# Kernel tuning notes

Measured on AMD Instinct MI355X. Metric: run time of the kernel, lower is better.

The kernel has to match this reference:

```python
import jax, jax.numpy as jnp
import numpy as np

N_NODES = 100000
N_EDGES = 1600000
IN_DIM = 64
OUT_DIM = 64


def setup_inputs() -> dict:
    key = jax.random.key(0)
    ks = jax.random.split(key, 8)
    features = jax.random.normal(ks[0], (N_NODES, IN_DIM), dtype=jnp.float32)
    q_w = jax.random.normal(ks[1], (IN_DIM, IN_DIM), dtype=jnp.float32) * 0.05
    q_b = jnp.zeros((IN_DIM,), dtype=jnp.float32)
    w_w = jax.random.normal(ks[2], (2 * IN_DIM, OUT_DIM), dtype=jnp.float32) * 0.05
    w_b = jnp.zeros((OUT_DIM,), dtype=jnp.float32)
    alpha = jax.random.uniform(ks[3], (N_EDGES,), dtype=jnp.float32)
    src = jax.random.randint(ks[4], (N_EDGES,), 0, N_NODES, dtype=jnp.int32)
    dst = jax.random.randint(ks[5], (N_EDGES,), 0, N_NODES, dtype=jnp.int32)
    return {"features": features, "q_w": q_w, "q_b": q_b,
            "w_w": w_w, "w_b": w_b, "alpha": alpha, "src": src, "dst": dst}


def reference(features, q_w, q_b, w_w, w_b, alpha, src, dst):
    # h = ReLU(q(features)) -- projected features for both src and dst nodes
    h = jax.nn.relu(features @ q_w + q_b)                      # [N, in_dim]
    # edge-weighted messages: u_mul_e('h','alpha') then sum by dst
    msgs = h[src] * alpha[:, None]                             # [E, in_dim]
    h_n = jax.ops.segment_sum(msgs, dst, num_segments=features.shape[0])  # [N, in_dim]
    # concat + linear + ReLU
    z = jax.nn.relu(jnp.concatenate([h, h_n], axis=-1) @ w_w + w_b)       # [N, out_dim]
    # L2 normalize (torch.norm default p=2)
    return z / jnp.linalg.norm(z, axis=-1, keepdims=True)
```

## Files before the change

kernel.cpp:

```cpp
#include <hip/hip_runtime.h>
#include <hip/hip_bf16.h>

#define IN_DIM 64
#define OUT_DIM 64

typedef float nt_f4 __attribute__((ext_vector_type(4)));

__global__ void canary_kernel(int* __restrict__ offsets, int n, int nE) {
    if (threadIdx.x == 0 && blockIdx.x == 0) offsets[n] = nE;
}

__global__ __launch_bounds__(256) void proj_kernel(
    const float4* __restrict__ feat4, const float4* __restrict__ qw4,
    const float4* __restrict__ qb4, float4* __restrict__ h4,
    int* __restrict__ counts, int n) {
    const size_t gtid = blockIdx.x * (size_t)256 + threadIdx.x;
    const int rg   = (int)(gtid >> 2);
    const int sub  = (int)(gtid & 3);
    const int row0 = rg * 4;
    if (row0 >= n) return;
    const int rmax = (n - row0 < 4) ? (n - row0) : 4;

    float4 acc[4][4];
    #pragma unroll
    for (int r = 0; r < 4; ++r)
        #pragma unroll
        for (int m = 0; m < 4; ++m) acc[r][m] = qb4[sub * 4 + m];

    for (int k4 = 0; k4 < 16; ++k4) {
        float4 xv[4];
        #pragma unroll
        for (int r = 0; r < 4; ++r) {
            const int rr = (r < rmax) ? r : 0;
            xv[r] = feat4[(size_t)(row0 + rr) * 16 + k4];
        }
        float4 w[4][4];
        #pragma unroll
        for (int j = 0; j < 4; ++j)
            #pragma unroll
            for (int m = 0; m < 4; ++m)
                w[j][m] = qw4[(k4 * 4 + j) * 16 + sub * 4 + m];
        #pragma unroll
        for (int j = 0; j < 4; ++j) {
            #pragma unroll
            for (int r = 0; r < 4; ++r) {
                const float xs = (j == 0) ? xv[r].x : (j == 1) ? xv[r].y
                               : (j == 2) ? xv[r].z : xv[r].w;
                #pragma unroll
                for (int m = 0; m < 4; ++m) {
                    acc[r][m].x = fmaf(xs, w[j][m].x, acc[r][m].x);
                    acc[r][m].y = fmaf(xs, w[j][m].y, acc[r][m].y);
                    acc[r][m].z = fmaf(xs, w[j][m].z, acc[r][m].z);
                    acc[r][m].w = fmaf(xs, w[j][m].w, acc[r][m].w);
                }
            }
        }
    }

    #pragma unroll
    for (int r = 0; r < 4; ++r) {
        if (r >= rmax) break;
        if (sub == 0) counts[row0 + r] = 0;
        #pragma unroll
        for (int m = 0; m < 4; ++m) {
            float4 v = acc[r][m];
            v.x = fmaxf(v.x, 0.f); v.y = fmaxf(v.y, 0.f);
            v.z = fmaxf(v.z, 0.f); v.w = fmaxf(v.w, 0.f);
            h4[(size_t)(row0 + r) * 16 + sub * 4 + m] = v;
        }
    }
}

__global__ __launch_bounds__(256) void count_kernel(
    const int* __restrict__ dst, int* __restrict__ counts, int n, int nE) {
    const int e = blockIdx.x * 256 + threadIdx.x;
    if (e >= nE) return;
    int d = __builtin_nontemporal_load(&dst[e]);
    d = ((unsigned)d < (unsigned)n) ? d : 0;
    atomicAdd(&counts[d], 1);
}

__global__ __launch_bounds__(256) void scan1_kernel(
    const int* __restrict__ counts, int* __restrict__ offsets,
    int* __restrict__ blocksums, int n) {
    __shared__ int s[256];
    const int tid = threadIdx.x;
    const int i = blockIdx.x * 256 + tid;
    const int v = (i < n) ? counts[i] : 0;
    s[tid] = v;
    __syncthreads();
    #pragma unroll
    for (int off = 1; off < 256; off <<= 1) {
        const int t = (tid >= off) ? s[tid - off] : 0;
        __syncthreads();
        s[tid] += t;
        __syncthreads();
    }
    if (i < n) offsets[i] = s[tid] - v;
    if (tid == 255) blocksums[blockIdx.x] = s[255];
}

__global__ __launch_bounds__(512) void scan2_kernel(int* __restrict__ blocksums, int nb) {
    __shared__ int s[512];
    const int tid = threadIdx.x;
    const int v = (tid < nb) ? blocksums[tid] : 0;
    s[tid] = v;
    __syncthreads();
    #pragma unroll
    for (int off = 1; off < 512; off <<= 1) {
        const int t = (tid >= off) ? s[tid - off] : 0;
        __syncthreads();
        s[tid] += t;
        __syncthreads();
    }
    if (tid < nb) blocksums[tid] = s[tid] - v;
}

__global__ __launch_bounds__(256) void scan3_kernel(
    int* __restrict__ offsets, int* __restrict__ cursor,
    const int* __restrict__ blocksums, int n, int nE) {
    const int i = blockIdx.x * 256 + threadIdx.x;
    if (i < n) {
        const int o = offsets[i] + blocksums[blockIdx.x];
        offsets[i] = o;
        cursor[i]  = o;
    }
    if (i == 0) offsets[n] = nE;
}

__global__ __launch_bounds__(256) void fill_kernel(
    const int* __restrict__ dst, const int* __restrict__ src,
    const float* __restrict__ alpha, int* __restrict__ cursor,
    int2* __restrict__ edges_s, int n, int nE) {
    const int e = blockIdx.x * 256 + threadIdx.x;
    if (e >= nE) return;
    int d = __builtin_nontemporal_load(&dst[e]);
    d = ((unsigned)d < (unsigned)n) ? d : 0;
    const int s = __builtin_nontemporal_load(&src[e]);
    const float a = __builtin_nontemporal_load(&alpha[e]);
    const int p = atomicAdd(&cursor[d], 1);
    if ((unsigned)p < (unsigned)nE) {
        edges_s[p] = make_int2(s, __float_as_int(a));
    }
}

__global__ __launch_bounds__(256) void agg_kernel(
    const float4* __restrict__ h4, const int2* __restrict__ edges_s,
    const int* __restrict__ offsets, float4* __restrict__ hn4, int n, int nE) {
    const size_t gtid = blockIdx.x * (size_t)256 + threadIdx.x;
    const int v    = (int)(gtid >> 6);
    const int lane = (int)(gtid & 63);
    const int q    = lane >> 4;
    const int c4   = lane & 15;
    if (v >= n) return;

    int b  = offsets[v];
    int e1 = offsets[v + 1];
    if (b < 0) b = 0;
    if (e1 > nE) e1 = nE;

    float4 acc = make_float4(0.f, 0.f, 0.f, 0.f);
    for (int j = b + q; j < e1; j += 4) {
        const int2 ed = edges_s[j];
        int s = ed.x;
        s = ((unsigned)s < (unsigned)n) ? s : 0;
        const float a = __int_as_float(ed.y);
        const float4 hv = h4[(size_t)s * 16 + c4];
        acc.x = fmaf(hv.x, a, acc.x);
        acc.y = fmaf(hv.y, a, acc.y);
        acc.z = fmaf(hv.z, a, acc.z);
        acc.w = fmaf(hv.w, a, acc.w);
    }
    acc.x += __shfl_xor(acc.x, 16, 64); acc.y += __shfl_xor(acc.y, 16, 64);
    acc.z += __shfl_xor(acc.z, 16, 64); acc.w += __shfl_xor(acc.w, 16, 64);
    acc.x += __shfl_xor(acc.x, 32, 64); acc.y += __shfl_xor(acc.y, 32, 64);
    acc.z += __shfl_xor(acc.z, 32, 64); acc.w += __shfl_xor(acc.w, 32, 64);

    if (q == 0) hn4[(size_t)v * 16 + c4] = acc;
}

__global__ __launch_bounds__(256) void zero_kernel(float* __restrict__ p, size_t cnt) {
    const size_t i = blockIdx.x * (size_t)256 + threadIdx.x;
    if (i < cnt) p[i] = 0.f;
}
__global__ __launch_bounds__(256) void scatter_kernel(
    const float4* __restrict__ h4, const float* __restrict__ alpha,
    const int* __restrict__ src, const int* __restrict__ dst,
    float* __restrict__ hn, int nE) {
    const size_t gtid = blockIdx.x * (size_t)256 + threadIdx.x;
    const int eid = (int)(gtid >> 4);
    const int c4  = (int)(gtid & 15);
    if (eid >= nE) return;
    const int   s = src[eid];
    const int   d = dst[eid];
    const float a = alpha[eid];
    const float4 v = h4[(size_t)s * 16 + c4];
    float* p = &hn[(size_t)d * IN_DIM + c4 * 4];
    unsafeAtomicAdd(p + 0, v.x * a);
    unsafeAtomicAdd(p + 1, v.y * a);
    unsafeAtomicAdd(p + 2, v.z * a);
    unsafeAtomicAdd(p + 3, v.w * a);
}

__global__ __launch_bounds__(256) void out_kernel(
    const float4* __restrict__ h4, const float4* __restrict__ hn4,
    const float4* __restrict__ ww4, const float4* __restrict__ wb4,
    float4* __restrict__ out4, int n) {
    const size_t gtid = blockIdx.x * (size_t)256 + threadIdx.x;
    const int rg   = (int)(gtid >> 2);
    const int sub  = (int)(gtid & 3);
    const int row0 = rg * 4;
    if (row0 >= n) return;
    const int rmax = (n - row0 < 4) ? (n - row0) : 4;

    float4 acc[4][4];
    #pragma unroll
    for (int r = 0; r < 4; ++r)
        #pragma unroll
        for (int m = 0; m < 4; ++m) acc[r][m] = wb4[sub * 4 + m];

    #pragma unroll
    for (int ph = 0; ph < 2; ++ph) {
        const float4* __restrict__ x4 = (ph == 0) ? h4 : hn4;
        for (int k4 = 0; k4 < 16; ++k4) {
            float4 xv[4];
            #pragma unroll
            for (int r = 0; r < 4; ++r) {
                const int rr = (r < rmax) ? r : 0;
                xv[r] = x4[(size_t)(row0 + rr) * 16 + k4];
            }
            float4 w[4][4];
            #pragma unroll
            for (int j = 0; j < 4; ++j)
                #pragma unroll
                for (int m = 0; m < 4; ++m)
                    w[j][m] = ww4[(ph * 64 + k4 * 4 + j) * 16 + sub * 4 + m];
            #pragma unroll
            for (int j = 0; j < 4; ++j) {
                #pragma unroll
                for (int r = 0; r < 4; ++r) {
                    const float xs = (j == 0) ? xv[r].x : (j == 1) ? xv[r].y
                                   : (j == 2) ? xv[r].z : xv[r].w;
                    #pragma unroll
                    for (int m = 0; m < 4; ++m) {
                        acc[r][m].x = fmaf(xs, w[j][m].x, acc[r][m].x);
                        acc[r][m].y = fmaf(xs, w[j][m].y, acc[r][m].y);
                        acc[r][m].z = fmaf(xs, w[j][m].z, acc[r][m].z);
                        acc[r][m].w = fmaf(xs, w[j][m].w, acc[r][m].w);
                    }
                }
            }
        }
    }

    float sq[4];
    #pragma unroll
    for (int r = 0; r < 4; ++r) {
        float s = 0.f;
        #pragma unroll
        for (int m = 0; m < 4; ++m) {
            acc[r][m].x = fmaxf(acc[r][m].x, 0.f);
            acc[r][m].y = fmaxf(acc[r][m].y, 0.f);
            acc[r][m].z = fmaxf(acc[r][m].z, 0.f);
            acc[r][m].w = fmaxf(acc[r][m].w, 0.f);
            s = fmaf(acc[r][m].x, acc[r][m].x, s);
            s = fmaf(acc[r][m].y, acc[r][m].y, s);
            s = fmaf(acc[r][m].z, acc[r][m].z, s);
            s = fmaf(acc[r][m].w, acc[r][m].w, s);
        }
        sq[r] = s;
    }
    #pragma unroll
    for (int r = 0; r < 4; ++r) {
        sq[r] += __shfl_xor(sq[r], 1, 64);
        sq[r] += __shfl_xor(sq[r], 2, 64);
    }

    #pragma unroll
    for (int r = 0; r < 4; ++r) {
        if (r >= rmax) break;
        const float inv = 1.0f / sqrtf(sq[r]);
        #pragma unroll
        for (int m = 0; m < 4; ++m) {
            nt_f4 v;
            v.x = acc[r][m].x * inv; v.y = acc[r][m].y * inv;
            v.z = acc[r][m].z * inv; v.w = acc[r][m].w * inv;
            __builtin_nontemporal_store(
                v, (nt_f4*)&out4[(size_t)(row0 + r) * 16 + sub * 4 + m]);
        }
    }
}

extern "C" void kernel_launch(void* const* d_in, const int* in_sizes, int n_in,
                              void* d_out, int out_size, void* d_ws, size_t ws_size,
                              hipStream_t stream) {
    const float* feat  = (const float*)d_in[0];
    const float* qw    = (const float*)d_in[1];
    const float* qb    = (const float*)d_in[2];
    const float* ww    = (const float*)d_in[3];
    const float* wb    = (const float*)d_in[4];
    const float* alpha = (const float*)d_in[5];
    const int*   src   = (const int*)d_in[6];
    const int*   dst   = (const int*)d_in[7];
    float* out = (float*)d_out;

    const int n  = in_sizes[0] / IN_DIM;
    const int nE = in_sizes[5];
    const int NB = (n + 255) / 256;

    float* h        = (float*)d_ws;
    float* hn       = h + (size_t)n * IN_DIM;
    int*   counts   = (int*)(hn + (size_t)n * IN_DIM);
    int*   offsets  = counts + n;
    int*   cursor   = offsets + (n + 1);
    int*   blocksums= cursor + n;
    char*  raw      = (char*)(blocksums + NB);
    int2*  edges_s  = (int2*)(((uintptr_t)raw + 7) & ~(uintptr_t)7);
    const size_t needed = (size_t)((char*)(edges_s + nE) - (char*)d_ws);
    const bool do_csr = ws_size >= needed;

    canary_kernel<<<1, 64, 0, stream>>>(offsets, n, nE);

    {
        const long long t = ((long long)(n + 3) / 4) * 4;
        proj_kernel<<<(int)((t + 255) / 256), 256, 0, stream>>>(
            (const float4*)feat, (const float4*)qw, (const float4*)qb,
            (float4*)h, counts, n);
    }

    if (do_csr) {
        count_kernel<<<(nE + 255) / 256, 256, 0, stream>>>(dst, counts, n, nE);
        scan1_kernel<<<NB, 256, 0, stream>>>(counts, offsets, blocksums, n);
        scan2_kernel<<<1, 512, 0, stream>>>(blocksums, NB);
        scan3_kernel<<<NB, 256, 0, stream>>>(offsets, cursor, blocksums, n, nE);
        fill_kernel<<<(nE + 255) / 256, 256, 0, stream>>>(
            dst, src, alpha, cursor, edges_s, n, nE);
        agg_kernel<<<(int)(((long long)n * 64 + 255) / 256), 256, 0, stream>>>(
            (const float4*)h, edges_s, offsets, (float4*)hn, n, nE);
    } else {
        const size_t cnt = (size_t)n * IN_DIM;
        zero_kernel<<<(int)((cnt + 255) / 256), 256, 0, stream>>>(hn, cnt);
        scatter_kernel<<<(int)(((long long)nE * 16 + 255) / 256), 256, 0, stream>>>(
            (const float4*)h, alpha, src, dst, hn, nE);
    }

    {
        const long long t = ((long long)(n + 3) / 4) * 4;
        out_kernel<<<(int)((t + 255) / 256), 256, 0, stream>>>(
            (const float4*)h, (const float4*)hn, (const float4*)ww,
            (const float4*)wb, (float4*)out, n);
    }
}
```

Baseline: 450.0 us.

## Two-pass bucketed partition for CSR fill to localize atomics and scatters

Replaces the single-pass edge fill with a two-stage partition. First, each block bins 4096 edges by coarse destination bucket (512 nodes per bucket) in shared memory and writes them contiguously into a temporary buffer, packing dst, src and a truncated alpha into 64 bits. A second pass then scatters from bucket-ordered records, so the per-node cursor atomics and edge writes hit localized memory regions. This adds an extra pass over the edges and a lossy alpha encoding (low 2 mantissa bits dropped, 17-bit indices). It also reuses the hn buffer as scratch and removes the nontemporal loads.

```diff
diff --git a/kernel.cpp b/kernel.cpp
--- a/kernel.cpp
+++ b/kernel.cpp
@@ -3,8 +3,11 @@
 
 #define IN_DIM 64
 #define OUT_DIM 64
+#define EPB 4096
+#define BSHIFT 9
 
 typedef float nt_f4 __attribute__((ext_vector_type(4)));
+typedef unsigned long long u64;
 
 __global__ void canary_kernel(int* __restrict__ offsets, int n, int nE) {
     if (threadIdx.x == 0 && blockIdx.x == 0) offsets[n] = nE;
@@ -75,7 +78,7 @@
     const int* __restrict__ dst, int* __restrict__ counts, int n, int nE) {
     const int e = blockIdx.x * 256 + threadIdx.x;
     if (e >= nE) return;
-    int d = __builtin_nontemporal_load(&dst[e]);
+    int d = dst[e];
     d = ((unsigned)d < (unsigned)n) ? d : 0;
     atomicAdd(&counts[d], 1);
 }
@@ -118,14 +121,93 @@
 
 __global__ __launch_bounds__(256) void scan3_kernel(
     int* __restrict__ offsets, int* __restrict__ cursor,
-    const int* __restrict__ blocksums, int n, int nE) {
+    const int* __restrict__ blocksums, int* __restrict__ bcur,
+    int n, int nE) {
     const int i = blockIdx.x * 256 + threadIdx.x;
     if (i < n) {
         const int o = offsets[i] + blocksums[blockIdx.x];
         offsets[i] = o;
         cursor[i]  = o;
+        if ((i & ((1 << BSHIFT) - 1)) == 0) bcur[i >> BSHIFT] = o;
     }
     if (i == 0) offsets[n] = nE;
+}
+
+__global__ __launch_bounds__(256) void partA_kernel(
+    const int* __restrict__ dst, const int* __restrict__ src,
+    const float* __restrict__ alpha, int* __restrict__ bcur,
+    u64* __restrict__ tmp, int n, int nE, int nbuk) {
+    __shared__ int hist[256];
+    __shared__ int lofs[256];
+    __shared__ int lcur[256];
+    __shared__ int gbase[256];
+    __shared__ u64 stage[EPB];
+    __shared__ unsigned short sbuk[EPB];
+
+    const int tid = threadIdx.x;
+    const int e0  = blockIdx.x * EPB;
+    const int cnt = (nE - e0 < EPB) ? (nE - e0) : EPB;
+
+    hist[tid] = 0;
+    __syncthreads();
+
+    for (int i = tid; i < cnt; i += 256) {
+        int d = dst[e0 + i];
+        d = ((unsigned)d < (unsigned)n) ? d : 0;
+        atomicAdd(&hist[d >> BSHIFT], 1);
+    }
+    __syncthreads();
+
+    const int v = hist[tid];
+    lofs[tid] = v;
+    __syncthreads();
+    #pragma unroll
+    for (int off = 1; off < 256; off <<= 1) {
+        const int t = (tid >= off) ? lofs[tid - off] : 0;
+        __syncthreads();
+        lofs[tid] += t;
+        __syncthreads();
+    }
+    const int excl = lofs[tid] - v;
+    __syncthreads();
+    lofs[tid] = excl;
+    lcur[tid] = excl;
+    if (tid < nbuk) gbase[tid] = atomicAdd(&bcur[tid], v);
+    __syncthreads();
+
+    for (int i = tid; i < cnt; i += 256) {
+        int d = dst[e0 + i];
+        d = ((unsigned)d < (unsigned)n) ? d : 0;
+        const int s = src[e0 + i];
+        const unsigned ab = __float_as_uint(alpha[e0 + i]) >> 2;
+        const int b = d >> BSHIFT;
+        int lp = atomicAdd(&lcur[b], 1);
+        lp = ((unsigned)lp < (unsigned)EPB) ? lp : 0;
+        stage[lp] = (u64)(d & 0x1FFFF) | ((u64)(s & 0x1FFFF) << 17)
+                  | ((u64)ab << 34);
+        sbuk[lp]  = (unsigned short)b;
+    }
+    __syncthreads();
+
+    for (int i = tid; i < cnt; i += 256) {
+        const int b = sbuk[i];
+        int d0 = gbase[b] + (i - lofs[b]);
+        if ((unsigned)d0 < (unsigned)nE) tmp[d0] = stage[i];
+    }
+}
+
+__global__ __launch_bounds__(256) void partB_kernel(
+    const u64* __restrict__ tmp, int* __restrict__ cursor,
+    int2* __restrict__ edges_s, int n, int nE) {
+    const int i = blockIdx.x * 256 + threadIdx.x;
+    if (i >= nE) return;
+    const u64 rec = tmp[i];
+    int d = (int)(rec & 0x1FFFF);
+    d = ((unsigned)d < (unsigned)n) ? d : 0;
+    const int s = (int)((rec >> 17) & 0x1FFFF);
+    const int ab = (int)((unsigned)(rec >> 34) << 2);
+    const int p = atomicAdd(&cursor[d], 1);
+    if ((unsigned)p < (unsigned)nE) edges_s[p] = make_int2(s, ab);
 }
 
 __global__ __launch_bounds__(256) void fill_kernel(
@@ -134,14 +216,12 @@
     int2* __restrict__ edges_s, int n, int nE) {
     const int e = blockIdx.x * 256 + threadIdx.x;
     if (e >= nE) return;
-    int d = __builtin_nontemporal_load(&dst[e]);
+    int d = dst[e];
     d = ((unsigned)d < (unsigned)n) ? d : 0;
-    const int s = __builtin_nontemporal_load(&src[e]);
-    const float a = __builtin_nontemporal_load(&alpha[e]);
+    const int s = src[e];
+    const float a = alpha[e];
     const int p = atomicAdd(&cursor[d], 1);
-    if ((unsigned)p < (unsigned)nE) {
-        edges_s[p] = make_int2(s, __float_as_int(a));
-    }
+    if ((unsigned)p < (unsigned)nE) edges_s[p] = make_int2(s, __float_as_int(a));
 }
 
 __global__ __launch_bounds__(256) void agg_kernel(
@@ -304,9 +384,10 @@
     const int*   dst   = (const int*)d_in[7];
     float* out = (float*)d_out;
 
-    const int n  = in_sizes[0] / IN_DIM;
-    const int nE = in_sizes[5];
-    const int NB = (n + 255) / 256;
+    const int n    = in_sizes[0] / IN_DIM;
+    const int nE   = in_sizes[5];
+    const int NB   = (n + 255) / 256;
+    const int NBUK = (n + (1 << BSHIFT) - 1) >> BSHIFT;
 
     float* h        = (float*)d_ws;
     float* hn       = h + (size_t)n * IN_DIM;
@@ -314,10 +395,12 @@
     int*   offsets  = counts + n;
     int*   cursor   = offsets + (n + 1);
     int*   blocksums= cursor + n;
-    char*  raw      = (char*)(blocksums + NB);
+    int*   bcur     = blocksums + NB;
+    char*  raw      = (char*)(bcur + NBUK);
     int2*  edges_s  = (int2*)(((uintptr_t)raw + 7) & ~(uintptr_t)7);
     const size_t needed = (size_t)((char*)(edges_s + nE) - (char*)d_ws);
     const bool do_csr = ws_size >= needed;
+    u64* tmp = (u64*)hn;
 
     canary_kernel<<<1, 64, 0, stream>>>(offsets, n, nE);
 
@@ -332,9 +415,17 @@
         count_kernel<<<(nE + 255) / 256, 256, 0, stream>>>(dst, counts, n, nE);
         scan1_kernel<<<NB, 256, 0, stream>>>(counts, offsets, blocksums, n);
         scan2_kernel<<<1, 512, 0, stream>>>(blocksums, NB);
-        scan3_kernel<<<NB, 256, 0, stream>>>(offsets, cursor, blocksums, n, nE);
-        fill_kernel<<<(nE + 255) / 256, 256, 0, stream>>>(
-            dst, src, alpha, cursor, edges_s, n, nE);
+        scan3_kernel<<<NB, 256, 0, stream>>>(offsets, cursor, blocksums, bcur, n, nE);
+        if (NBUK <= 256) {
+            const int NBA = (nE + EPB - 1) / EPB;
+            partA_kernel<<<NBA, 256, 0, stream>>>(
+                dst, src, alpha, bcur, tmp, n, nE, NBUK);
+            partB_kernel<<<(nE + 255) / 256, 256, 0, stream>>>(
+                tmp, cursor, edges_s, n, nE);
+        } else {
+            fill_kernel<<<(nE + 255) / 256, 256, 0, stream>>>(
+                dst, src, alpha, cursor, edges_s, n, nE);
+        }
         agg_kernel<<<(int)(((long long)n * 64 + 255) / 256), 256, 0, stream>>>(
             (const float4*)h, edges_s, offsets, (float4*)hn, n, nE);
     } else {
```

Measured after the change: 443.6 us. About the same (-1.4%).
